# Optimization experiments

Measured on AMD Instinct MI355X. Metric: run time of the kernel, lower is better.

The kernel has to match this reference:

```python
import jax, jax.numpy as jnp
import numpy as np

N = 100000          # nodes
E = 1600000         # edges (avg degree 16)
IN_F = 256          # in_features
OUT_F = 128         # out_features


def setup_inputs() -> dict:
    key = jax.random.key(0)
    k1, k2, k3, k4, k5 = jax.random.split(key, 5)
    x = jax.random.normal(k1, (N, IN_F), dtype=jnp.float32)
    edge_index = jax.random.randint(k2, (2, E), 0, N, dtype=jnp.int32)
    # xavier_uniform-style init (gain 1.414)
    def xav(k, shape):
        fan_in, fan_out = shape[0], shape[1]
        bound = 1.414 * np.sqrt(6.0 / (fan_in + fan_out))
        return jax.random.uniform(k, shape, jnp.float32, -bound, bound)
    W = xav(k3, (IN_F, OUT_F))
    a = xav(k4, (2 * OUT_F, 1))
    W_em = xav(k5, (IN_F, OUT_F))
    return {"x": x, "edge_index": edge_index, "W": W, "a": a, "W_em": W_em}


def reference(x, edge_index, W, a, W_em):
    # DisGALayer.forward_sparse, att_type=1, gnn_type='AT', eval mode (dropout off)
    src = edge_index[0]
    dst = edge_index[1]
    h = x @ W                                   # [N, OUT_F]
    # edge_e = cat(h[src], h[dst]) @ a  ==  h[src]@a_src + h[dst]@a_dst
    a_src, a_dst = a[:OUT_F], a[OUT_F:]
    edge_e = h[src] @ a_src + h[dst] @ a_dst    # [E, 1]
    edge_ob = jax.nn.sigmoid(edge_e)            # [E, 1]
    # sp_softmax: softmax of edge values grouped by row (src)
    v = jnp.exp(edge_ob - jax.lax.stop_gradient(edge_ob.max()))
    denom = jax.ops.segment_sum(v, src, num_segments=N)   # [N, 1]
    attention = v / denom[src]                  # [E, 1]
    # sp_matmul: h_prime[i] = sum_{e: src(e)=i} att_e * h_em[dst(e)]
    h_em = x @ W_em                             # [N, OUT_F]
    h_prime = jax.ops.segment_sum(attention * h_em[dst], src, num_segments=N)
    return h_prime, edge_e
```

## Files before the change

kernel.cpp:

```cpp
#include <hip/hip_runtime.h>
#include <hip/hip_bf16.h>

#define NN 100000
#define NE 1600000
#define INF 256
#define OUTF 128
#define NBK ((NN + 127) / 128)
#define CHUNK 4096
#define NBA ((NE + CHUNK - 1) / CHUNK)
#define NGRP (NN / 32)
#define SCAP 6144
#define NMM 391

typedef __attribute__((ext_vector_type(8))) short short8;
typedef __attribute__((ext_vector_type(4))) float f32x4;
typedef __attribute__((ext_vector_type(4))) uint u32x4;

static __device__ __forceinline__ short f2bf(float f) {
    __hip_bfloat16 h = __float2bfloat16(f);
    return *reinterpret_cast<short*>(&h);
}

__global__ void k_setup(const float* __restrict__ W, const float* __restrict__ a,
                        const float* __restrict__ Wem, const int* __restrict__ src,
                        float* __restrict__ wsv, float* __restrict__ wdv,
                        ushort* __restrict__ Bsw, int* __restrict__ cntA) {
    const int b = blockIdx.x, t = threadIdx.x;
    if (b == 0) {
        const float* Wr = W + (size_t)t * OUTF;
        float sa = 0.f, sb = 0.f;
        #pragma unroll 8
        for (int k = 0; k < OUTF; ++k) {
            float w = Wr[k];
            sa += w * a[k];
            sb += w * a[OUTF + k];
        }
        wsv[t] = sa;
        wdv[t] = sb;
    } else if (b <= 8) {
        const int kt = b - 1;
        for (int idx = t; idx < 4096; idx += 256) {
            const int ct = idx >> 9;
            const int lane = (idx >> 3) & 63;
            const int j = idx & 7;
            const int k = kt * 32 + (lane >> 4) * 8 + j;
            const int c = ct * 16 + (lane & 15);
            Bsw[((size_t)(kt * 8 + ct) * 64 + lane) * 8 + j] =
                (ushort)f2bf(Wem[(size_t)k * OUTF + c]);
        }
    } else {
        __shared__ int cnt[NBK];
        const int c = b - 9;
        const int e0 = c * CHUNK;
        for (int i = t; i < NBK; i += 256) cnt[i] = 0;
        __syncthreads();
        for (int i = t; i < CHUNK; i += 256) {
            const int e = e0 + i;
            if (e < NE) atomicAdd(&cnt[src[e] >> 7], 1);
        }
        __syncthreads();
        for (int i = t; i < NBK; i += 256) cntA[(size_t)c * NBK + i] = cnt[i];
    }
}

__global__ __launch_bounds__(1024) void k_mmcs(
    const float* __restrict__ x, const ushort* __restrict__ Bsw,
    const float* __restrict__ wsv, const float* __restrict__ wdv,
    const int* __restrict__ cntA,
    float* __restrict__ s1, float* __restrict__ s2,
    char* __restrict__ hem8, float* __restrict__ scaleA,
    int* __restrict__ baseA, int* __restrict__ bsumB) {
    __shared__ ushort bswl[32768];
    const int b = blockIdx.x;
    const int t = threadIdx.x;
    if (b < NMM) {
        {
            const u32x4* gs = reinterpret_cast<const u32x4*>(Bsw);
            u32x4* ls = reinterpret_cast<u32x4*>(bswl);
            #pragma unroll
            for (int i = 0; i < 4; ++i) ls[t + i * 1024] = gs[t + i * 1024];
        }
        __syncthreads();

        const int w = t >> 6, lane = t & 63;
        const int rowbase = b * 256 + w * 16;
        const int r0 = lane & 15, kq = lane >> 4;
        const int row = rowbase + r0;
        const int rowc = (row < NN) ? row : NN - 1;
        const float* xp = x + (size_t)rowc * INF + kq * 8;

        f32x4 acc[8];
        #pragma unroll
        for (int ct = 0; ct < 8; ++ct) acc[ct] = (f32x4){0.f, 0.f, 0.f, 0.f};
        float sa = 0.f, sb = 0.f;

        #pragma unroll
        for (int kt = 0; kt < 8; ++kt) {
            const float4 a0 = *reinterpret_cast<const float4*>(xp + kt * 32);
            const float4 a1 = *reinterpret_cast<const float4*>(xp + kt * 32 + 4);
            const float4 w0 = *reinterpret_cast<const float4*>(wsv + kt * 32 + kq * 8);
            const float4 w1 = *reinterpret_cast<const float4*>(wsv + kt * 32 + kq * 8 + 4);
            const float4 u0 = *reinterpret_cast<const float4*>(wdv + kt * 32 + kq * 8);
            const float4 u1 = *reinterpret_cast<const float4*>(wdv + kt * 32 + kq * 8 + 4);
            sa += a0.x * w0.x + a0.y * w0.y + a0.z * w0.z + a0.w * w0.w
                + a1.x * w1.x + a1.y * w1.y + a1.z * w1.z + a1.w * w1.w;
            sb += a0.x * u0.x + a0.y * u0.y + a0.z * u0.z + a0.w * u0.w
                + a1.x * u1.x + a1.y * u1.y + a1.z * u1.z + a1.w * u1.w;
            short8 af;
            af[0] = f2bf(a0.x); af[1] = f2bf(a0.y); af[2] = f2bf(a0.z); af[3] = f2bf(a0.w);
            af[4] = f2bf(a1.x); af[5] = f2bf(a1.y); af[6] = f2bf(a1.z); af[7] = f2bf(a1.w);
            #pragma unroll
            for (int ct = 0; ct < 8; ++ct) {
                const short8 bf = *reinterpret_cast<const short8*>(
                    &bswl[((kt * 8 + ct) * 64 + lane) * 8]);
                acc[ct] = __builtin_amdgcn_mfma_f32_16x16x32_bf16(af, bf, acc[ct], 0, 0, 0);
            }
        }

        sa += __shfl_xor(sa, 16); sa += __shfl_xor(sa, 32);
        sb += __shfl_xor(sb, 16); sb += __shfl_xor(sb, 32);
        if (kq == 0 && row < NN) { s1[row] = sa; s2[row] = sb; }

        float mx[4];
        #pragma unroll
        for (int i = 0; i < 4; ++i) {
            float m = 0.f;
            #pragma unroll
            for (int ct = 0; ct < 8; ++ct) m = fmaxf(m, fabsf(acc[ct][i]));
            m = fmaxf(m, __shfl_xor(m, 1));
            m = fmaxf(m, __shfl_xor(m, 2));
            m = fmaxf(m, __shfl_xor(m, 4));
            m = fmaxf(m, __shfl_xor(m, 8));
            mx[i] = m;
        }
        #pragma unroll
        for (int i = 0; i < 4; ++i) {
            const int rr = rowbase + kq * 4 + i;
            const float inv = (mx[i] > 0.f) ? 127.f / mx[i] : 0.f;
            if (r0 == 0 && rr < NN) scaleA[rr] = mx[i];
            #pragma unroll
            for (int ct = 0; ct < 8; ++ct) {
                int q = (int)rintf(acc[ct][i] * inv);
                q = (q > 127) ? 127 : ((q < -127) ? -127 : q);
                uint p = (uint)(q & 255);
                p |= ((uint)__shfl_xor((int)p, 1) & 255u) << 8;
                uint word = p | ((uint)__shfl_xor((int)p, 2) << 16);
                if ((r0 & 3) == 0 && rr < NN) {
                    *reinterpret_cast<uint*>(
                        hem8 + ((size_t)(ct >> 1) * NN + rr) * 32
                             + (ct & 1) * 16 + r0) = word;
                }
            }
        }
    } else {
        int* sm = reinterpret_cast<int*>(bswl);
        const int bb = b - NMM;
        const int v = (t < NBA) ? cntA[(size_t)t * NBK + bb] : 0;
        sm[t] = v;
        __syncthreads();
        for (int off = 1; off < 1024; off <<= 1) {
            const int add = (t >= off) ? sm[t - off] : 0;
            __syncthreads();
            sm[t] += add;
            __syncthreads();
        }
        if (t < NBA) baseA[(size_t)t * NBK + bb] = sm[t] - v;
        if (t == 1023) bsumB[bb] = sm[1023];
    }
}

__global__ __launch_bounds__(1024) void k_bbase(
    const int* __restrict__ bsumB, int* __restrict__ bbase,
    int* __restrict__ offs) {
    __shared__ int sm[1024];
    const int t = threadIdx.x;
    const int v = (t < NBK) ? bsumB[t] : 0;
    sm[t] = v;
    __syncthreads();
    for (int off = 1; off < 1024; off <<= 1) {
        const int add = (t >= off) ? sm[t - off] : 0;
        __syncthreads();
        sm[t] += add;
        __syncthreads();
    }
    if (t < NBK) bbase[t] = sm[t] - v;
    if (t == 0) { bbase[NBK] = NE; offs[NN] = NE; }
}

__global__ __launch_bounds__(256) void k_binA(
    const int* __restrict__ src, const int* __restrict__ dst,
    const float* __restrict__ s1, const float* __restrict__ s2,
    float* __restrict__ ee_out, const int* __restrict__ bbase,
    const int* __restrict__ baseA, int2* __restrict__ ebA) {
    __shared__ int base[NBK];
    __shared__ int cnt[NBK];
    const int t = threadIdx.x;
    const int c = blockIdx.x;
    const int e0 = c * CHUNK;
    for (int i = t; i < NBK; i += 256) {
        base[i] = bbase[i] + baseA[(size_t)c * NBK + i];
        cnt[i] = 0;
    }
    __syncthreads();
    for (int i = t; i < CHUNK; i += 256) {
        const int e = e0 + i;
        if (e < NE) {
            const int s = src[e], d = dst[e];
            const float ee = s1[s] + s2[d];
            __builtin_nontemporal_store(ee, ee_out + e);
            const float ob = 1.f / (1.f + __expf(-ee));
            const float v = __expf(ob);
            int vq = (int)((v - 1.f) * 16384.f + 0.5f);
            vq = (vq > 32767) ? 32767 : vq;
            const int bk = s >> 7;
            const int r = atomicAdd(&cnt[bk], 1);
            ebA[base[bk] + r] = make_int2((d << 7) | (s & 127), vq);
        }
    }
}

__global__ __launch_bounds__(256) void k_sortB(
    const int* __restrict__ bbase, const int2* __restrict__ ebA,
    const float* __restrict__ scaleA,
    uint* __restrict__ ebB, int* __restrict__ offs) {
    __shared__ uint rx[SCAP];
    __shared__ ushort ry[SCAP];
    __shared__ int cnt[128];
    __shared__ int sum[128];
    __shared__ int sm[128];
    __shared__ int cur[128];
    __shared__ float fsl[128];
    const int b = blockIdx.x, t = threadIdx.x;
    const int n0 = b << 7;
    const int lo = bbase[b];
    const int hi = bbase[b + 1];
    const int n = hi - lo;
    if (t < 128) { cnt[t] = 0; sum[t] = 0; }
    __syncthreads();
    for (int i = t; i < n; i += 256) {
        const int2 r = ebA[lo + i];
        if (i < SCAP) { rx[i] = (uint)r.x; ry[i] = (ushort)r.y; }
        const int sidx = r.x & 127;
        atomicAdd(&cnt[sidx], 1);
        atomicAdd(&sum[sidx], r.y);
    }
    __syncthreads();
    const int v = (t < 128) ? cnt[t] : 0;
    if (t < 128) sm[t] = v;
    __syncthreads();
    for (int off = 1; off < 128; off <<= 1) {
        int add = 0;
        if (t < 128 && t >= off) add = sm[t - off];
        __syncthreads();
        if (t < 128) sm[t] += add;
        __syncthreads();
    }
    if (t < 128) {
        const int excl = sm[t] - v;
        cur[t] = excl;
        const int node = n0 + t;
        if (node < NN) offs[node] = lo + excl;
        fsl[t] = (v > 0) ? 1.f / (float)(v * 16384 + sum[t]) : 0.f;
    }
    __syncthreads();
    for (int i = t; i < n; i += 256) {
        uint x;
        int y;
        if (i < SCAP) { x = rx[i]; y = (int)ry[i]; }
        else { const int2 r = ebA[lo + i]; x = (uint)r.x; y = r.y; }
        const int sidx = x & 127;
        const uint d = x >> 7;
        const float att = (float)(16384 + y) * fsl[sidx];
        const float w = att * scaleA[d];
        int wq = (int)(w * 1024.f + 0.5f);
        wq = (wq > 32767) ? 32767 : wq;
        const int p = atomicAdd(&cur[sidx], 1);
        ebB[lo + p] = (d << 15) | (uint)wq;
    }
}

__global__ __launch_bounds__(256) void k_aggregate(
    const uint* __restrict__ eb, const int* __restrict__ offs,
    const char* __restrict__ hem8, float* __restrict__ out0) {
    const int slice = blockIdx.x & 3;
    const int grp = blockIdx.x >> 2;
    const int t = threadIdx.x;
    const int node = grp * 32 + (t >> 3);
    const int f = t & 7;
    const char* base = hem8 + (size_t)slice * NN * 32 + f * 4;
    const int beg = offs[node];
    const int end = offs[node + 1];

    int a0 = 0, a1 = 0, a2 = 0, a3 = 0;
    int j = beg;
    for (; j + 4 <= end; j += 4) {
        const uint r0 = eb[j];
        const uint r1 = eb[j + 1];
        const uint r2 = eb[j + 2];
        const uint r3 = eb[j + 3];
        const int w0 = (int)(r0 & 0x7fffu);
        const int w1 = (int)(r1 & 0x7fffu);
        const int w2 = (int)(r2 & 0x7fffu);
        const int w3 = (int)(r3 & 0x7fffu);
        const uint u0 = *reinterpret_cast<const uint*>(base + ((size_t)(r0 >> 15)) * 32);
        const uint u1 = *reinterpret_cast<const uint*>(base + ((size_t)(r1 >> 15)) * 32);
        const uint u2 = *reinterpret_cast<const uint*>(base + ((size_t)(r2 >> 15)) * 32);
        const uint u3 = *reinterpret_cast<const uint*>(base + ((size_t)(r3 >> 15)) * 32);
        a0 += w0 * (((int)(u0 << 24)) >> 24) + w1 * (((int)(u1 << 24)) >> 24)
            + w2 * (((int)(u2 << 24)) >> 24) + w3 * (((int)(u3 << 24)) >> 24);
        a1 += w0 * (((int)(u0 << 16)) >> 24) + w1 * (((int)(u1 << 16)) >> 24)
            + w2 * (((int)(u2 << 16)) >> 24) + w3 * (((int)(u3 << 16)) >> 24);
        a2 += w0 * (((int)(u0 << 8)) >> 24) + w1 * (((int)(u1 << 8)) >> 24)
            + w2 * (((int)(u2 << 8)) >> 24) + w3 * (((int)(u3 << 8)) >> 24);
        a3 += w0 * (((int)u0) >> 24) + w1 * (((int)u1) >> 24)
            + w2 * (((int)u2) >> 24) + w3 * (((int)u3) >> 24);
    }
    for (; j < end; ++j) {
        const uint r0 = eb[j];
        const int w0 = (int)(r0 & 0x7fffu);
        const uint u0 = *reinterpret_cast<const uint*>(base + ((size_t)(r0 >> 15)) * 32);
        a0 += w0 * (((int)(u0 << 24)) >> 24);
        a1 += w0 * (((int)(u0 << 16)) >> 24);
        a2 += w0 * (((int)(u0 << 8)) >> 24);
        a3 += w0 * (((int)u0) >> 24);
    }
    const float s = 1.f / (1024.f * 127.f);
    f32x4 o = {a0 * s, a1 * s, a2 * s, a3 * s};
    *reinterpret_cast<f32x4*>(
        out0 + (size_t)node * OUTF + slice * 32 + f * 4) = o;
}

extern "C" void kernel_launch(void* const* d_in, const int* in_sizes, int n_in,
                              void* d_out, int out_size, void* d_ws, size_t ws_size,
                              hipStream_t stream) {
    const float* x   = (const float*)d_in[0];
    const int* eidx  = (const int*)d_in[1];
    const float* W   = (const float*)d_in[2];
    const float* a   = (const float*)d_in[3];
    const float* Wem = (const float*)d_in[4];

    const int* src = eidx;
    const int* dst = eidx + NE;

    float* out0 = (float*)d_out;
    float* out1 = out0 + (size_t)NN * OUTF;

    float* wsv    = (float*)d_ws;
    float* wdv    = wsv + 256;
    float* s1     = wdv + 256;
    float* s2     = s1 + NN;
    float* scaleA = s2 + NN;
    ushort* Bsw   = (ushort*)(scaleA + NN);
    int* offs     = (int*)(Bsw + 32768);
    int* bsumB    = offs + NN + 4;
    int* bbase    = bsumB + 784;
    int* cntA     = bbase + 788;
    int* baseA    = cntA + NBA * NBK;
    int2* ebA     = (int2*)(baseA + NBA * NBK);
    uint* ebB     = (uint*)(ebA + NE);
    char* hem8    = (char*)(ebB + NE);

    hipLaunchKernelGGL(k_setup, dim3(9 + NBA), dim3(256), 0, stream,
                       W, a, Wem, src, wsv, wdv, Bsw, cntA);
    hipLaunchKernelGGL(k_mmcs, dim3(NMM + NBK), dim3(1024), 0, stream,
                       x, Bsw, wsv, wdv, cntA, s1, s2, hem8, scaleA,
                       baseA, bsumB);
    hipLaunchKernelGGL(k_bbase, dim3(1), dim3(1024), 0, stream, bsumB, bbase, offs);
    hipLaunchKernelGGL(k_binA, dim3(NBA), dim3(256), 0, stream,
                       src, dst, s1, s2, out1, bbase, baseA, ebA);
    hipLaunchKernelGGL(k_sortB, dim3(NBK), dim3(256), 0, stream,
                       bbase, ebA, scaleA, ebB, offs);
    hipLaunchKernelGGL(k_aggregate, dim3(4 * NGRP), dim3(256), 0, stream,
                       ebB, offs, hem8, out0);
}
```

Baseline: 148.6 us.

## Precompute bf16 x and attention dot products in setup kernel blocks

Adds conversion blocks to the setup kernel that cast x to bf16 and compute s1/s2 per-node scores, with each block recomputing the W·a vectors into shared memory. The matmul kernel then loads pre-converted bf16 rows and drops the fp32 loads, conversion and dot-product work. This shortens the matmul inner loop and may overlap the conversion with edge counting. In exchange it adds an extra write and re-read of a half-size copy of x, plus redundant W·a work in every conversion block.

New measurement: 285.5 us. 1.92x slower.

```diff
diff --git a/kernel.cpp b/kernel.cpp
--- a/kernel.cpp
+++ b/kernel.cpp
@@ -11,6 +11,7 @@
 #define NGRP (NN / 32)
 #define SCAP 6144
 #define NMM 391
+#define NCONV 1563
 
 typedef __attribute__((ext_vector_type(8))) short short8;
 typedef __attribute__((ext_vector_type(4))) float f32x4;
@@ -23,22 +24,13 @@
 
 __global__ void k_setup(const float* __restrict__ W, const float* __restrict__ a,
                         const float* __restrict__ Wem, const int* __restrict__ src,
-                        float* __restrict__ wsv, float* __restrict__ wdv,
-                        ushort* __restrict__ Bsw, int* __restrict__ cntA) {
+                        const float* __restrict__ x,
+                        ushort* __restrict__ Bsw, int* __restrict__ cntA,
+                        ushort* __restrict__ xbf,
+                        float* __restrict__ s1, float* __restrict__ s2) {
     const int b = blockIdx.x, t = threadIdx.x;
-    if (b == 0) {
-        const float* Wr = W + (size_t)t * OUTF;
-        float sa = 0.f, sb = 0.f;
-        #pragma unroll 8
-        for (int k = 0; k < OUTF; ++k) {
-            float w = Wr[k];
-            sa += w * a[k];
-            sb += w * a[OUTF + k];
-        }
-        wsv[t] = sa;
-        wdv[t] = sb;
-    } else if (b <= 8) {
-        const int kt = b - 1;
+    if (b < 8) {
+        const int kt = b;
         for (int idx = t; idx < 4096; idx += 256) {
             const int ct = idx >> 9;
             const int lane = (idx >> 3) & 63;
@@ -48,9 +40,9 @@
             Bsw[((size_t)(kt * 8 + ct) * 64 + lane) * 8 + j] =
                 (ushort)f2bf(Wem[(size_t)k * OUTF + c]);
         }
-    } else {
+    } else if (b < 8 + NBA) {
         __shared__ int cnt[NBK];
-        const int c = b - 9;
+        const int c = b - 8;
         const int e0 = c * CHUNK;
         for (int i = t; i < NBK; i += 256) cnt[i] = 0;
         __syncthreads();
@@ -60,14 +52,56 @@
         }
         __syncthreads();
         for (int i = t; i < NBK; i += 256) cntA[(size_t)c * NBK + i] = cnt[i];
+    } else {
+        __shared__ float lwsv[256];
+        __shared__ float lwdv[256];
+        {
+            const float* Wr = W + (size_t)t * OUTF;
+            float pa = 0.f, pb = 0.f;
+            #pragma unroll 8
+            for (int k = 0; k < OUTF; ++k) {
+                const float w = Wr[k];
+                pa += w * a[k];
+                pb += w * a[OUTF + k];
+            }
+            lwsv[t] = pa;
+            lwdv[t] = pb;
+        }
+        __syncthreads();
+        const int cb = b - 8 - NBA;
+        const int row = cb * 64 + (t >> 2);
+        const int q = t & 3;
+        const int rowc = (row < NN) ? row : NN - 1;
+        const float* xp = x + (size_t)rowc * INF + q * 64;
+        float sa = 0.f, sb = 0.f;
+        #pragma unroll
+        for (int i = 0; i < 8; ++i) {
+            const float4 v0 = *reinterpret_cast<const float4*>(xp + i * 8);
+            const float4 v1 = *reinterpret_cast<const float4*>(xp + i * 8 + 4);
+            const int e = q * 64 + i * 8;
+            sa += v0.x * lwsv[e]     + v0.y * lwsv[e + 1]
+                + v0.z * lwsv[e + 2] + v0.w * lwsv[e + 3]
+                + v1.x * lwsv[e + 4] + v1.y * lwsv[e + 5]
+                + v1.z * lwsv[e + 6] + v1.w * lwsv[e + 7];
+            sb += v0.x * lwdv[e]     + v0.y * lwdv[e + 1]
+                + v0.z * lwdv[e + 2] + v0.w * lwdv[e + 3]
+                + v1.x * lwdv[e + 4] + v1.y * lwdv[e + 5]
+                + v1.z * lwdv[e + 6] + v1.w * lwdv[e + 7];
+            short8 o;
+            o[0] = f2bf(v0.x); o[1] = f2bf(v0.y); o[2] = f2bf(v0.z); o[3] = f2bf(v0.w);
+            o[4] = f2bf(v1.x); o[5] = f2bf(v1.y); o[6] = f2bf(v1.z); o[7] = f2bf(v1.w);
+            if (row < NN)
+                *reinterpret_cast<short8*>(xbf + (size_t)row * INF + e) = o;
+        }
+        sa += __shfl_xor(sa, 1); sa += __shfl_xor(sa, 2);
+        sb += __shfl_xor(sb, 1); sb += __shfl_xor(sb, 2);
+        if (q == 0 && row < NN) { s1[row] = sa; s2[row] = sb; }
     }
 }
 
 __global__ __launch_bounds__(1024) void k_mmcs(
-    const float* __restrict__ x, const ushort* __restrict__ Bsw,
-    const float* __restrict__ wsv, const float* __restrict__ wdv,
+    const ushort* __restrict__ xbf, const ushort* __restrict__ Bsw,
     const int* __restrict__ cntA,
-    float* __restrict__ s1, float* __restrict__ s2,
     char* __restrict__ hem8, float* __restrict__ scaleA,
     int* __restrict__ baseA, int* __restrict__ bsumB) {
     __shared__ ushort bswl[32768];
@@ -87,28 +121,16 @@
         const int r0 = lane & 15, kq = lane >> 4;
         const int row = rowbase + r0;
         const int rowc = (row < NN) ? row : NN - 1;
-        const float* xp = x + (size_t)rowc * INF + kq * 8;
+        const short8* xp = reinterpret_cast<const short8*>(
+            xbf + (size_t)rowc * INF);
 
         f32x4 acc[8];
         #pragma unroll
         for (int ct = 0; ct < 8; ++ct) acc[ct] = (f32x4){0.f, 0.f, 0.f, 0.f};
-        float sa = 0.f, sb = 0.f;
 
         #pragma unroll
         for (int kt = 0; kt < 8; ++kt) {
-            const float4 a0 = *reinterpret_cast<const float4*>(xp + kt * 32);
-            const float4 a1 = *reinterpret_cast<const float4*>(xp + kt * 32 + 4);
-            const float4 w0 = *reinterpret_cast<const float4*>(wsv + kt * 32 + kq * 8);
-            const float4 w1 = *reinterpret_cast<const float4*>(wsv + kt * 32 + kq * 8 + 4);
-            const float4 u0 = *reinterpret_cast<const float4*>(wdv + kt * 32 + kq * 8);
-            const float4 u1 = *reinterpret_cast<const float4*>(wdv + kt * 32 + kq * 8 + 4);
-            sa += a0.x * w0.x + a0.y * w0.y + a0.z * w0.z + a0.w * w0.w
-                + a1.x * w1.x + a1.y * w1.y + a1.z * w1.z + a1.w * w1.w;
-            sb += a0.x * u0.x + a0.y * u0.y + a0.z * u0.z + a0.w * u0.w
-                + a1.x * u1.x + a1.y * u1.y + a1.z * u1.z + a1.w * u1.w;
-            short8 af;
-            af[0] = f2bf(a0.x); af[1] = f2bf(a0.y); af[2] = f2bf(a0.z); af[3] = f2bf(a0.w);
-            af[4] = f2bf(a1.x); af[5] = f2bf(a1.y); af[6] = f2bf(a1.z); af[7] = f2bf(a1.w);
+            const short8 af = xp[kt * 4 + kq];
             #pragma unroll
             for (int ct = 0; ct < 8; ++ct) {
                 const short8 bf = *reinterpret_cast<const short8*>(
@@ -116,10 +138,6 @@
                 acc[ct] = __builtin_amdgcn_mfma_f32_16x16x32_bf16(af, bf, acc[ct], 0, 0, 0);
             }
         }
-
-        sa += __shfl_xor(sa, 16); sa += __shfl_xor(sa, 32);
-        sb += __shfl_xor(sb, 16); sb += __shfl_xor(sb, 32);
-        if (kq == 0 && row < NN) { s1[row] = sa; s2[row] = sb; }
 
         float mx[4];
         #pragma unroll
@@ -345,9 +363,7 @@
     float* out0 = (float*)d_out;
     float* out1 = out0 + (size_t)NN * OUTF;
 
-    float* wsv    = (float*)d_ws;
-    float* wdv    = wsv + 256;
-    float* s1     = wdv + 256;
+    float* s1     = (float*)d_ws;
     float* s2     = s1 + NN;
     float* scaleA = s2 + NN;
     ushort* Bsw   = (ushort*)(scaleA + NN);
@@ -359,12 +375,12 @@
     int2* ebA     = (int2*)(baseA + NBA * NBK);
     uint* ebB     = (uint*)(ebA + NE);
     char* hem8    = (char*)(ebB + NE);
-
-    hipLaunchKernelGGL(k_setup, dim3(9 + NBA), dim3(256), 0, stream,
-                       W, a, Wem, src, wsv, wdv, Bsw, cntA);
+    ushort* xbf   = (ushort*)(hem8 + (size_t)NN * OUTF);
+
+    hipLaunchKernelGGL(k_setup, dim3(8 + NBA + NCONV), dim3(256), 0, stream,
+                       W, a, Wem, src, x, Bsw, cntA, xbf, s1, s2);
     hipLaunchKernelGGL(k_mmcs, dim3(NMM + NBK), dim3(1024), 0, stream,
-                       x, Bsw, wsv, wdv, cntA, s1, s2, hem8, scaleA,
-                       baseA, bsumB);
+                       xbf, Bsw, cntA, hem8, scaleA, baseA, bsumB);
     hipLaunchKernelGGL(k_bbase, dim3(1), dim3(1024), 0, stream, bsumB, bbase, offs);
     hipLaunchKernelGGL(k_binA, dim3(NBA), dim3(256), 0, stream,
                        src, dst, s1, s2, out1, bbase, baseA, ebA);
```
